# Kernel tuning notes

Hardware: AMD Instinct MI355X
Metric: run time of the kernel (lower is better)

## Reference

```python
import jax, jax.numpy as jnp
import numpy as np

C = 256          # channels
K = 7            # kernel_size
GC = 16          # group_channels
G = C // GC      # groups = 16
R = 4            # reduction_ratio
CR = C // R      # reduced channels = 64
EPS = 1e-5


def setup_inputs() -> dict:
    key = jax.random.key(0)
    ks = jax.random.split(key, 8)
    B, H, W = 8, 56, 56
    x = jax.random.normal(ks[0], (B, C, H, W), dtype=jnp.float32)
    # conv1: 1x1, C -> C//R
    W1 = jax.random.normal(ks[1], (CR, C), dtype=jnp.float32) * (1.0 / np.sqrt(C))
    b1 = jax.random.normal(ks[2], (CR,), dtype=jnp.float32) * 0.01
    # batchnorm (eval-mode) params
    gamma = jnp.ones((CR,), dtype=jnp.float32)
    beta = jnp.zeros((CR,), dtype=jnp.float32)
    mean = jax.random.normal(ks[3], (CR,), dtype=jnp.float32) * 0.1
    var = jax.random.uniform(ks[4], (CR,), dtype=jnp.float32, minval=0.5, maxval=1.5)
    # conv2: 1x1, C//R -> K*K*G
    W2 = jax.random.normal(ks[5], (K * K * G, CR), dtype=jnp.float32) * (1.0 / np.sqrt(CR))
    b2 = jax.random.normal(ks[6], (K * K * G,), dtype=jnp.float32) * 0.01
    return {"x": x, "W1": W1, "b1": b1, "gamma": gamma, "beta": beta,
            "mean": mean, "var": var, "W2": W2, "b2": b2}


def reference(x, W1, b1, gamma, beta, mean, var, W2, b2):
    B, _, H, Wd = x.shape
    pad = (K - 1) // 2
    # --- weight generation branch: conv1 -> BN(eval) -> ReLU -> conv2 ---
    y = jnp.einsum('bchw,oc->bohw', x, W1) + b1[None, :, None, None]
    y = (y - mean[None, :, None, None]) * (gamma[None, :, None, None]
        * jax.lax.rsqrt(var + EPS)[None, :, None, None]) + beta[None, :, None, None]
    y = jax.nn.relu(y)
    wgt = jnp.einsum('bchw,oc->bohw', y, W2) + b2[None, :, None, None]  # (B, G*K*K, H, W)
    wgt = wgt.reshape(B, G, K * K, H, Wd)
    # --- unfold: gather KxK neighborhoods (stride=1, same padding) ---
    xp = jnp.pad(x, ((0, 0), (0, 0), (pad, pad), (pad, pad)))
    # (B, C, K*K, H, W); kernel positions ordered row-major like nn.Unfold
    patches = jnp.stack([xp[:, :, i:i + H, j:j + Wd]
                         for i in range(K) for j in range(K)], axis=2)
    patches = patches.reshape(B, G, GC, K * K, H, Wd)
    # --- per-pixel weighted sum over kernel window ---
    out = jnp.einsum('bgckhw,bgkhw->bgchw', patches, wgt)
    return out.reshape(B, C, H, Wd)
```

## Files before the change

kernel.cpp:

```cpp
#include <hip/hip_runtime.h>
#include <hip/hip_bf16.h>

#define CCH   256
#define NG    16
#define GCN   16
#define CRD   64
#define HH    56
#define WWD   56
#define HWP   3136
#define BB    8
#define NPIX  25088
#define PADW  62
#define PADHW 3844
#define K2    49
#define O2N   784
#define EPSV  1e-5f

typedef unsigned short ushort_t;
typedef __attribute__((ext_vector_type(8))) short bf16x8;
typedef __attribute__((ext_vector_type(4))) float f32x4;

#define XP_OFF   0
#define XP_SZ    7872512
#define XT_OFF   7872512
#define YT_OFF   11083776
#define W1B_OFF  11886592
#define W2B_OFF  11894784
#define B2P_OFF  11920384
#define BNS_OFF  11921184
#define BNT_OFF  11921248

__device__ __forceinline__ ushort_t f2bf(float f) {
    unsigned u = __builtin_bit_cast(unsigned, f);
    return (ushort_t)((u + 0x7FFFu + ((u >> 16) & 1u)) >> 16);
}

__global__ __launch_bounds__(256) void prep_kernel(const float* __restrict__ W1,
                                                   const float* __restrict__ b1,
                                                   const float* __restrict__ gamma,
                                                   const float* __restrict__ beta,
                                                   const float* __restrict__ mean,
                                                   const float* __restrict__ var,
                                                   const float* __restrict__ W2,
                                                   const float* __restrict__ b2,
                                                   float* __restrict__ ws) {
    int gid = blockIdx.x * 256 + threadIdx.x;
    int stride = gridDim.x * 256;
    uint4 z = {0u, 0u, 0u, 0u};
    uint4* xpv = (uint4*)(ws + XP_OFF);
    for (int e = gid; e < XP_SZ / 4; e += stride) xpv[e] = z;

    ushort_t* w1b = (ushort_t*)(ws + W1B_OFF);
    if (gid < CRD * CCH) w1b[gid] = f2bf(W1[gid]);
    ushort_t* w2b = (ushort_t*)(ws + W2B_OFF);
    if (gid < 800 * CRD) w2b[gid] = (gid < O2N * CRD) ? f2bf(W2[gid]) : (ushort_t)0;
    if (gid < 800) ws[B2P_OFF + gid] = (gid < O2N) ? b2[gid] : 0.f;
    if (gid < CRD) {
        float s = gamma[gid] * rsqrtf(var[gid] + EPSV);
        ws[BNS_OFF + gid] = s;
        ws[BNT_OFF + gid] = (b1[gid] - mean[gid]) * s + beta[gid];
    }
}

__global__ __launch_bounds__(256) void pack_x(const float* __restrict__ x,
                                              float* __restrict__ ws) {
    __shared__ ushort_t st[64 * 270];
    int tid = threadIdx.x;
    int b = blockIdx.y, hw0 = blockIdx.x * 64;
    int lane = tid & 63, c4 = tid >> 6;
    int hw = hw0 + lane;
    int h = hw / WWD, w = hw - h * WWD;
    const float* xb = x + (b * CCH) * HWP + hw;
    float* xpd = ws + XP_OFF + (b * CCH) * PADHW + (h + 3) * PADW + (w + 3);
#pragma unroll 8
    for (int i = 0; i < 64; ++i) {
        int c = i * 4 + c4;
        float v = xb[c * HWP];
        st[lane * 270 + c] = f2bf(v);
        xpd[c * PADHW] = v;
    }
    __syncthreads();
    const unsigned* stu = (const unsigned*)st;
    unsigned* xtu = (unsigned*)(ws + XT_OFF);
    int rowg = b * HWP + hw0;
#pragma unroll
    for (int k = 0; k < 32; ++k) {
        int idx = k * 256 + tid;
        int row = idx >> 7, c2 = idx & 127;
        xtu[(rowg + row) * 128 + c2] = stu[row * 135 + c2];
    }
}

__global__ __launch_bounds__(256) void conv1_mfma(float* __restrict__ ws) {
    const ushort_t* xt  = (const ushort_t*)(ws + XT_OFF);
    const ushort_t* w1b = (const ushort_t*)(ws + W1B_OFF);
    const float* bns = ws + BNS_OFF;
    const float* bnt = ws + BNT_OFF;
    ushort_t* yt = (ushort_t*)(ws + YT_OFF);

    int tid = threadIdx.x, lane = tid & 63, wv = tid >> 6;
    int lr = lane & 15, lg = lane >> 4;
    int ot = blockIdx.x;
    int pixbase = blockIdx.y * 128 + wv * 32;

    const bf16x8* ap = (const bf16x8*)(w1b + (ot * 16 + lr) * CCH + lg * 8);
    bf16x8 a[8];
#pragma unroll
    for (int ks = 0; ks < 8; ++ks) a[ks] = ap[ks * 4];

    f32x4 acc[2] = {{0.f,0.f,0.f,0.f}, {0.f,0.f,0.f,0.f}};
#pragma unroll
    for (int f = 0; f < 2; ++f) {
        const bf16x8* bp = (const bf16x8*)(xt + (pixbase + f * 16 + lr) * CCH + lg * 8);
#pragma unroll
        for (int ks = 0; ks < 8; ++ks)
            acc[f] = __builtin_amdgcn_mfma_f32_16x16x32_bf16(a[ks], bp[ks * 4], acc[f], 0, 0, 0);
    }

    int o0 = ot * 16 + lg * 4;
    float4 s4 = *(const float4*)(bns + o0);
    float4 t4 = *(const float4*)(bnt + o0);
#pragma unroll
    for (int f = 0; f < 2; ++f) {
        int pix = pixbase + f * 16 + lr;
        union { ushort_t u[4]; uint2 v; } pk;
        pk.u[0] = f2bf(fmaxf(acc[f][0] * s4.x + t4.x, 0.f));
        pk.u[1] = f2bf(fmaxf(acc[f][1] * s4.y + t4.y, 0.f));
        pk.u[2] = f2bf(fmaxf(acc[f][2] * s4.z + t4.z, 0.f));
        pk.u[3] = f2bf(fmaxf(acc[f][3] * s4.w + t4.w, 0.f));
        *(uint2*)(yt + pix * CRD + o0) = pk.v;
    }
}

__global__ __launch_bounds__(256, 4) void invol_fused(const float* __restrict__ ws,
                                                      float* __restrict__ out) {
    __shared__ uint4 lds4[1792];
    unsigned char* ldsb = (unsigned char*)lds4;

    int h0t = blockIdx.x;
    int g   = blockIdx.y;
    int b   = blockIdx.z;
    int tid = threadIdx.x, lane = tid & 63, wv = tid >> 6;
    int lr = lane & 15, lg = lane >> 4;
    int pix0 = b * HWP + h0t * 224;

    const uint4* ysrc = (const uint4*)((const ushort_t*)(ws + YT_OFF) + pix0 * CRD);
    for (int i = tid; i < 1792; i += 256) {
        int row = i >> 3;
        unsigned off = (unsigned)(i * 16) ^ (unsigned)((row & 7) << 4);
        *(uint4*)(ldsb + off) = ysrc[i];
    }
    __syncthreads();

    const ushort_t* w2b = (const ushort_t*)(ws + W2B_OFF);
    const bf16x8* ar = (const bf16x8*)(w2b + (g * K2 + wv * 16 + lr) * CRD);
    bf16x8 a0 = ar[lg], a1 = ar[4 + lg];

    f32x4 acc[14];
#pragma unroll
    for (int pt = 0; pt < 14; ++pt) acc[pt] = (f32x4){0.f, 0.f, 0.f, 0.f};
#pragma unroll
    for (int pt = 0; pt < 14; ++pt) {
        int row = pt * 16 + lr;
        unsigned sw = (unsigned)((row & 7) << 4);
        uint4 b0 = *(const uint4*)(ldsb + ((unsigned)(row * 128 + lg * 16) ^ sw));
        uint4 b1 = *(const uint4*)(ldsb + ((unsigned)(row * 128 + 64 + lg * 16) ^ sw));
        acc[pt] = __builtin_amdgcn_mfma_f32_16x16x32_bf16(a0, __builtin_bit_cast(bf16x8, b0), acc[pt], 0, 0, 0);
        acc[pt] = __builtin_amdgcn_mfma_f32_16x16x32_bf16(a1, __builtin_bit_cast(bf16x8, b1), acc[pt], 0, 0, 0);
    }
    __syncthreads();

    ushort_t* wl = (ushort_t*)ldsb;
    const float* b2p = ws + B2P_OFF;
    float b2v[4];
#pragma unroll
    for (int j = 0; j < 4; ++j) {
        int k = wv * 16 + lg * 4 + j;
        b2v[j] = b2p[g * K2 + k];
    }
#pragma unroll
    for (int pt = 0; pt < 14; ++pt) {
        int pix = pt * 16 + lr;
        int r = pix / WWD;
        int w = pix - r * WWD;
#pragma unroll
        for (int j = 0; j < 4; ++j) {
            int k = wv * 16 + lg * 4 + j;
            if (k < K2) {
                int ki = k / 7, dj = k - ki * 7;
                wl[(((ki * 4 + r) * WWD + w) << 3) + dj] = f2bf(acc[pt][j] + b2v[j]);
            }
        }
    }
    __syncthreads();

    int w = lane, cq = wv;
    if (w < WWD) {
        const float* xpb = ws + XP_OFF + (b * CCH + g * GCN + cq * 4) * PADHW
                         + h0t * 4 * PADW + w;
        float acc2[4][4];
#pragma unroll
        for (int c = 0; c < 4; ++c)
#pragma unroll
            for (int r = 0; r < 4; ++r) acc2[c][r] = 0.f;

        const unsigned char* wbase = ldsb + w * 16;
#pragma unroll
        for (int xr = 0; xr < 10; ++xr) {
            float xv[4][8];
#pragma unroll
            for (int c = 0; c < 4; ++c)
                __builtin_memcpy(&xv[c][0], xpb + c * PADHW + xr * PADW, 32);
#pragma unroll
            for (int ki = 0; ki < 7; ++ki) {
                int r = xr - ki;
                if (r >= 0 && r < 4) {
                    uint4 q = *(const uint4*)(wbase + (ki * 4 + r) * (WWD * 16));
                    unsigned uu[4] = {q.x, q.y, q.z, q.w};
                    float wf[8];
#pragma unroll
                    for (int t = 0; t < 4; ++t) {
                        wf[2 * t]     = __builtin_bit_cast(float, uu[t] << 16);
                        wf[2 * t + 1] = __builtin_bit_cast(float, uu[t] & 0xffff0000u);
                    }
#pragma unroll
                    for (int dj = 0; dj < 7; ++dj)
#pragma unroll
                        for (int c = 0; c < 4; ++c)
                            acc2[c][r] = fmaf(xv[c][dj], wf[dj], acc2[c][r]);
                }
            }
        }

#pragma unroll
        for (int c = 0; c < 4; ++c)
#pragma unroll
            for (int r = 0; r < 4; ++r)
                out[(b * CCH + g * GCN + cq * 4 + c) * HWP + (h0t * 4 + r) * WWD + w]
                    = acc2[c][r];
    }
}

extern "C" void kernel_launch(void* const* d_in, const int* in_sizes, int n_in,
                              void* d_out, int out_size, void* d_ws, size_t ws_size,
                              hipStream_t stream) {
    const float* x     = (const float*)d_in[0];
    const float* W1    = (const float*)d_in[1];
    const float* b1    = (const float*)d_in[2];
    const float* gamma = (const float*)d_in[3];
    const float* beta  = (const float*)d_in[4];
    const float* mean  = (const float*)d_in[5];
    const float* var   = (const float*)d_in[6];
    const float* W2    = (const float*)d_in[7];
    const float* b2    = (const float*)d_in[8];

    float* ws  = (float*)d_ws;
    float* out = (float*)d_out;

    prep_kernel<<<2048, 256, 0, stream>>>(W1, b1, gamma, beta, mean, var, W2, b2, ws);
    pack_x<<<dim3(HWP / 64, BB), 256, 0, stream>>>(x, ws);
    conv1_mfma<<<dim3(4, NPIX / 128), 256, 0, stream>>>(ws);
    invol_fused<<<dim3(14, NG, BB), 256, 0, stream>>>(ws, out);
}
```

Baseline: 72.58 us.

## Remap involution thread work to 4-pixel strips with fp32 LDS weights

```diff
diff --git a/kernel.cpp b/kernel.cpp
--- a/kernel.cpp
+++ b/kernel.cpp
@@ -10,25 +10,27 @@
 #define HWP   3136
 #define BB    8
 #define NPIX  25088
-#define PADW  62
-#define PADHW 3844
 #define K2    49
 #define O2N   784
 #define EPSV  1e-5f
 
+#define XROWS 62
+#define XRW   64
+#define CHSTR 3968
+
 typedef unsigned short ushort_t;
 typedef __attribute__((ext_vector_type(8))) short bf16x8;
 typedef __attribute__((ext_vector_type(4))) float f32x4;
 
 #define XP_OFF   0
-#define XP_SZ    7872512
-#define XT_OFF   7872512
-#define YT_OFF   11083776
-#define W1B_OFF  11886592
-#define W2B_OFF  11894784
-#define B2P_OFF  11920384
-#define BNS_OFF  11921184
-#define BNT_OFF  11921248
+#define XP2_SZ   8126464
+#define XT_OFF   8126464
+#define YT_OFF   11337728
+#define W1B_OFF  12140544
+#define W2B_OFF  12148736
+#define B2P_OFF  12174336
+#define BNS_OFF  12175136
+#define BNT_OFF  12175200
 
 __device__ __forceinline__ ushort_t f2bf(float f) {
     unsigned u = __builtin_bit_cast(unsigned, f);
@@ -48,7 +50,7 @@
     int stride = gridDim.x * 256;
     uint4 z = {0u, 0u, 0u, 0u};
     uint4* xpv = (uint4*)(ws + XP_OFF);
-    for (int e = gid; e < XP_SZ / 4; e += stride) xpv[e] = z;
+    for (int e = gid; e < XP2_SZ / 4; e += stride) xpv[e] = z;
 
     ushort_t* w1b = (ushort_t*)(ws + W1B_OFF);
     if (gid < CRD * CCH) w1b[gid] = f2bf(W1[gid]);
@@ -71,13 +73,13 @@
     int hw = hw0 + lane;
     int h = hw / WWD, w = hw - h * WWD;
     const float* xb = x + (b * CCH) * HWP + hw;
-    float* xpd = ws + XP_OFF + (b * CCH) * PADHW + (h + 3) * PADW + (w + 3);
+    float* xpd = ws + XP_OFF + (size_t)(b * CCH) * CHSTR + (h + 3) * XRW + (w + 3);
 #pragma unroll 8
     for (int i = 0; i < 64; ++i) {
         int c = i * 4 + c4;
         float v = xb[c * HWP];
         st[lane * 270 + c] = f2bf(v);
-        xpd[c * PADHW] = v;
+        xpd[c * CHSTR] = v;
     }
     __syncthreads();
     const unsigned* stu = (const unsigned*)st;
@@ -132,9 +134,9 @@
     }
 }
 
-__global__ __launch_bounds__(256, 4) void invol_fused(const float* __restrict__ ws,
+__global__ __launch_bounds__(256, 3) void invol_fused(const float* __restrict__ ws,
                                                       float* __restrict__ out) {
-    __shared__ uint4 lds4[1792];
+    __shared__ uint4 lds4[2744];
     unsigned char* ldsb = (unsigned char*)lds4;
 
     int h0t = blockIdx.x;
@@ -144,7 +146,7 @@
     int lr = lane & 15, lg = lane >> 4;
     int pix0 = b * HWP + h0t * 224;
 
-    const uint4* ysrc = (const uint4*)((const ushort_t*)(ws + YT_OFF) + pix0 * CRD);
+    const uint4* ysrc = (const uint4*)((const ushort_t*)(ws + YT_OFF) + (size_t)pix0 * CRD);
     for (int i = tid; i < 1792; i += 256) {
         int row = i >> 3;
         unsigned off = (unsigned)(i * 16) ^ (unsigned)((row & 7) << 4);
@@ -170,74 +172,82 @@
     }
     __syncthreads();
 
-    ushort_t* wl = (ushort_t*)ldsb;
+    float* wlf = (float*)ldsb;
     const float* b2p = ws + B2P_OFF;
     float b2v[4];
 #pragma unroll
-    for (int j = 0; j < 4; ++j) {
-        int k = wv * 16 + lg * 4 + j;
-        b2v[j] = b2p[g * K2 + k];
-    }
+    for (int j = 0; j < 4; ++j)
+        b2v[j] = b2p[g * K2 + wv * 16 + lg * 4 + j];
 #pragma unroll
     for (int pt = 0; pt < 14; ++pt) {
         int pix = pt * 16 + lr;
         int r = pix / WWD;
         int w = pix - r * WWD;
+        int wb = w >> 2, t = w & 3;
+        int base = wb * 16 + ((r ^ (wb & 3)) << 2) + t;
 #pragma unroll
         for (int j = 0; j < 4; ++j) {
             int k = wv * 16 + lg * 4 + j;
-            if (k < K2) {
-                int ki = k / 7, dj = k - ki * 7;
-                wl[(((ki * 4 + r) * WWD + w) << 3) + dj] = f2bf(acc[pt][j] + b2v[j]);
+            if (k < K2)
+                wlf[k * 224 + base] = acc[pt][j] + b2v[j];
+        }
+    }
+    __syncthreads();
+
+    int c4 = lane >> 4, wb = lane & 15;
+    if (wb < 14) {
+        int ch = g * GCN + wv * 4 + c4;
+        const float* xrb = ws + XP_OFF + (size_t)(b * CCH + ch) * CHSTR
+                         + (h0t * 4) * XRW + wb * 4;
+
+        float xw[5][12];
+#pragma unroll
+        for (int n = 0; n < 4; ++n) {
+            __builtin_memcpy(&xw[n][0], xrb + n * XRW, 16);
+            __builtin_memcpy(&xw[n][4], xrb + n * XRW + 4, 16);
+            __builtin_memcpy(&xw[n][8], xrb + n * XRW + 8, 16);
+        }
+
+        float acc2[4][4];
+#pragma unroll
+        for (int r = 0; r < 4; ++r)
+#pragma unroll
+            for (int t = 0; t < 4; ++t) acc2[r][t] = 0.f;
+
+        int swz = (wb & 3) << 2;
+#pragma unroll
+        for (int ki = 0; ki < 7; ++ki) {
+            if (ki < 6) {
+                int n = ki + 4;
+                float* dst = &xw[n % 5][0];
+                __builtin_memcpy(dst,     xrb + n * XRW, 16);
+                __builtin_memcpy(dst + 4, xrb + n * XRW + 4, 16);
+                __builtin_memcpy(dst + 8, xrb + n * XRW + 8, 16);
             }
-        }
-    }
-    __syncthreads();
-
-    int w = lane, cq = wv;
-    if (w < WWD) {
-        const float* xpb = ws + XP_OFF + (b * CCH + g * GCN + cq * 4) * PADHW
-                         + h0t * 4 * PADW + w;
-        float acc2[4][4];
-#pragma unroll
-        for (int c = 0; c < 4; ++c)
-#pragma unroll
-            for (int r = 0; r < 4; ++r) acc2[c][r] = 0.f;
-
-        const unsigned char* wbase = ldsb + w * 16;
-#pragma unroll
-        for (int xr = 0; xr < 10; ++xr) {
-            float xv[4][8];
-#pragma unroll
-            for (int c = 0; c < 4; ++c)
-                __builtin_memcpy(&xv[c][0], xpb + c * PADHW + xr * PADW, 32);
-#pragma unroll
-            for (int ki = 0; ki < 7; ++ki) {
-                int r = xr - ki;
-                if (r >= 0 && r < 4) {
-                    uint4 q = *(const uint4*)(wbase + (ki * 4 + r) * (WWD * 16));
-                    unsigned uu[4] = {q.x, q.y, q.z, q.w};
-                    float wf[8];
-#pragma unroll
-                    for (int t = 0; t < 4; ++t) {
-                        wf[2 * t]     = __builtin_bit_cast(float, uu[t] << 16);
-                        wf[2 * t + 1] = __builtin_bit_cast(float, uu[t] & 0xffff0000u);
-                    }
-#pragma unroll
-                    for (int dj = 0; dj < 7; ++dj)
-#pragma unroll
-                        for (int c = 0; c < 4; ++c)
-                            acc2[c][r] = fmaf(xv[c][dj], wf[dj], acc2[c][r]);
+#pragma unroll
+            for (int dj = 0; dj < 7; ++dj) {
+                int k = ki * 7 + dj;
+                const float* kb = wlf + k * 224 + wb * 16;
+                f32x4 wr0 = *(const f32x4*)(kb + ((0 << 2) ^ swz));
+                f32x4 wr1 = *(const f32x4*)(kb + ((1 << 2) ^ swz));
+                f32x4 wr2 = *(const f32x4*)(kb + ((2 << 2) ^ swz));
+                f32x4 wr3 = *(const f32x4*)(kb + ((3 << 2) ^ swz));
+#pragma unroll
+                for (int t = 0; t < 4; ++t) {
+                    acc2[0][t] = fmaf(xw[(ki + 0) % 5][t + dj], wr0[t], acc2[0][t]);
+                    acc2[1][t] = fmaf(xw[(ki + 1) % 5][t + dj], wr1[t], acc2[1][t]);
+                    acc2[2][t] = fmaf(xw[(ki + 2) % 5][t + dj], wr2[t], acc2[2][t]);
+                    acc2[3][t] = fmaf(xw[(ki + 3) % 5][t + dj], wr3[t], acc2[3][t]);
                 }
             }
         }
 
-#pragma unroll
-        for (int c = 0; c < 4; ++c)
-#pragma unroll
-            for (int r = 0; r < 4; ++r)
-                out[(b * CCH + g * GCN + cq * 4 + c) * HWP + (h0t * 4 + r) * WWD + w]
-                    = acc2[c][r];
+        float* ob = out + (size_t)(b * CCH + ch) * HWP + (h0t * 4) * WWD + wb * 4;
+#pragma unroll
+        for (int r = 0; r < 4; ++r) {
+            float4 v = {acc2[r][0], acc2[r][1], acc2[r][2], acc2[r][3]};
+            *(float4*)(ob + r * WWD) = v;
+        }
     }
 }
 
```

Result: slower. 101.7 us (+40.1%).
